# Performance work log

Measured on AMD Instinct MI355X. Metric: run time of the kernel, lower is better.

## Reference

```python
import jax, jax.numpy as jnp
import numpy as np

N = 100000   # nodes
E = 1600000  # edges (avg degree 16)
D = 128      # feature dim
L = 2        # nr_layers


def setup_inputs() -> dict:
    key = jax.random.key(0)
    k0, k1, k2, k3, k4 = jax.random.split(key, 5)
    x = jax.random.normal(k0, (N, D), dtype=jnp.float32)
    edge_index = jax.random.randint(k1, (2, E), 0, N, dtype=jnp.int32)
    edge_weight = jax.random.uniform(k2, (E,), dtype=jnp.float32)
    scale = 1.0 / np.sqrt(D)
    W_self = jax.random.normal(k3, (L, D, D), dtype=jnp.float32) * scale
    W_neigh = jax.random.normal(k4, (L, D, D), dtype=jnp.float32) * scale
    bias = jnp.zeros((L, D), dtype=jnp.float32)
    return {"x": x, "edge_index": edge_index, "edge_weight": edge_weight,
            "W_self": W_self, "W_neigh": W_neigh, "bias": bias}


def reference(x, edge_index, edge_weight, W_self, W_neigh, bias):
    src, dst = edge_index[0], edge_index[1]
    n = x.shape[0]
    # mean-aggregation denominator: number of incoming edges per node
    deg = jax.ops.segment_sum(jnp.ones_like(edge_weight), dst, num_segments=n)
    deg = jnp.maximum(deg, 1.0)[:, None]  # [N,1]
    nl = W_self.shape[0]
    for l in range(nl):
        msg = edge_weight[:, None] * x[src]                       # [E,D] gather
        agg = jax.ops.segment_sum(msg, dst, num_segments=n) / deg  # [N,D] scatter
        x = agg @ W_neigh[l] + x @ W_self[l] + bias[l]
        x = jax.nn.relu(x) if l < nl - 1 else jax.nn.sigmoid(x)
    return x
```

## Files before the change

### kernel.cpp

```cpp
#include <hip/hip_runtime.h>
#include <math.h>


#define D 128
#define BK_SHIFT 9
#define BK_NODES 512
#define CAP 10240
#define CH1 2048

typedef unsigned int uint;
typedef unsigned short ushort;
typedef __attribute__((ext_vector_type(2))) _Float16 h2;
typedef __attribute__((ext_vector_type(8))) _Float16 half8;
typedef __attribute__((ext_vector_type(4))) float f32x4;

__device__ __forceinline__ uint pkrtz(float lo, float hi) {
    auto v = __builtin_amdgcn_cvt_pkrtz(lo, hi);
    union { decltype(v) h; uint u; } c;
    c.h = v;
    return c.u;
}
__device__ __forceinline__ ushort f2h(float f) {
    return (ushort)(pkrtz(f, f) & 0xffffu);
}
__device__ __forceinline__ h2 u2h(uint u) {
    union { uint u; h2 h; } c;
    c.u = u;
    return c.h;
}
__device__ __forceinline__ uint h2u(h2 h) {
    union { h2 h; uint u; } c;
    c.h = h;
    return c.u;
}

__global__ __launch_bounds__(256) void k_prep(
    const float* __restrict__ x, uint* __restrict__ xh, int n8,
    const float* __restrict__ Wn, const float* __restrict__ Ws,
    ushort* __restrict__ wt, int wtotal,
    const int* __restrict__ src, const int* __restrict__ dst,
    const float* __restrict__ w, int E,
    int* __restrict__ bcur, int2* __restrict__ bedge,
    int nbSort, int nbConv)
{
    __shared__ int h[256];
    __shared__ int gbase[256];
    const int t = threadIdx.x;
    const int bid = blockIdx.x;

    if (bid >= nbSort) {
        int cb = bid - nbSort;
        if (cb < nbConv) {
            int i = cb * 256 + t;
            if (i >= n8) return;
            const float4* p = reinterpret_cast<const float4*>(x + (size_t)i * 8);
            float4 a = p[0], b = p[1];
            uint4 o;
            o.x = pkrtz(a.x, a.y);
            o.y = pkrtz(a.z, a.w);
            o.z = pkrtz(b.x, b.y);
            o.w = pkrtz(b.z, b.w);
            reinterpret_cast<uint4*>(xh)[i] = o;
        } else {
            int idx = (cb - nbConv) * 256 + t;
            if (idx >= wtotal) return;
            int l = idx >> 15;
            int j = (idx >> 8) & 127;
            int k = idx & 255;
            float v = (k < 128) ? Wn[(size_t)l * 16384 + (size_t)k * 128 + j]
                                : Ws[(size_t)l * 16384 + (size_t)(k - 128) * 128 + j];
            wt[idx] = f2h(v);
        }
        return;
    }

    h[t] = 0;
    __syncthreads();
    const int base0 = bid * CH1;
    uint pk[8]; float wr[8]; int br[8];
#pragma unroll
    for (int j = 0; j < 8; ++j) {
        int i = base0 + j * 256 + t;
        br[j] = -1;
        if (i < E) {
            int d = dst[i];
            int b = d >> BK_SHIFT;
            int r = atomicAdd(&h[b], 1);
            pk[j] = (uint)src[i] | ((uint)(d & (BK_NODES - 1)) << 17);
            wr[j] = w[i];
            br[j] = (b << 16) | r;
        }
    }
    __syncthreads();
    if (h[t] > 0) gbase[t] = atomicAdd(&bcur[t], h[t]);
    __syncthreads();
#pragma unroll
    for (int j = 0; j < 8; ++j) {
        if (br[j] >= 0) {
            int b = br[j] >> 16, r = br[j] & 0xffff;
            int slot = gbase[b] + r;
            if (slot < CAP)
                bedge[(size_t)b * CAP + slot] = make_int2((int)pk[j], __float_as_int(wr[j]));
        }
    }
}

__global__ __launch_bounds__(512) void k_sort2(
    const int2* __restrict__ bedge, const int* __restrict__ bcnt,
    int N, int2* __restrict__ rsdeg, int2* __restrict__ srcw)
{
    __shared__ int h[512];
    __shared__ int sa[512];
    __shared__ int sb[512];
    __shared__ int cur[512];
    const int t = threadIdx.x;
    const int b = blockIdx.x;
    const int gb = b * CAP;
    int cnt = bcnt[b];
    if (cnt > CAP) cnt = CAP;
    const int lo = b << BK_SHIFT;
    h[t] = 0;
    __syncthreads();
    for (int i = t; i < cnt; i += 512) {
        atomicAdd(&h[((uint)bedge[gb + i].x >> 17) & 511], 1);
    }
    __syncthreads();
    sa[t] = h[t];
    __syncthreads();
    int* sin = sa; int* sout = sb;
    for (int off = 1; off < 512; off <<= 1) {
        int v = sin[t];
        if (t >= off) v += sin[t - off];
        sout[t] = v;
        __syncthreads();
        int* tmp = sin; sin = sout; sout = tmp;
    }
    const int ex = sin[t] - h[t];
    cur[t] = ex;
    if (lo + t < N) rsdeg[lo + t] = make_int2(gb + ex, h[t]);
    __syncthreads();
    for (int i = t; i < cnt; i += 512) {
        int2 pe = bedge[gb + i];
        int n9 = ((uint)pe.x >> 17) & 511;
        int off = atomicAdd(&cur[n9], 1);
        float wv = __int_as_float(pe.y);
        srcw[gb + off] = make_int2((pe.x & 0x1FFFF) << 8, (int)pkrtz(wv, wv));
    }
}

__global__ __launch_bounds__(256, 8) void k_agg(
    const uint* __restrict__ xh,
    const int2* __restrict__ srcw,
    const int2* __restrict__ rsdeg,
    uint* __restrict__ agg, int N)
{
    const int tid = threadIdx.x;
    const int wv = tid >> 6;
    const int lane = tid & 63;
    const int node = blockIdx.x * 4 + wv;
    if (node >= N) return;
    const int q = lane >> 3;
    const int c8 = lane & 7;
    const int2 rd = rsdeg[node];
    const int st = rd.x;
    const int num = rd.y;
    const int en = st + num;

    h2 a2[8];
#pragma unroll
    for (int j = 0; j < 8; ++j) a2[j] = u2h(0u);

#pragma unroll 2
    for (int e = st + q; e < en; e += 8) {
        const int2 sw = srcw[e];
        const h2 w2 = u2h((uint)sw.y);
        const char* rowp = (const char*)xh + (uint)sw.x + (c8 << 5);
        const uint4 v0 = *reinterpret_cast<const uint4*>(rowp);
        const uint4 v1 = *reinterpret_cast<const uint4*>(rowp + 16);
        a2[0] = __builtin_elementwise_fma(w2, u2h(v0.x), a2[0]);
        a2[1] = __builtin_elementwise_fma(w2, u2h(v0.y), a2[1]);
        a2[2] = __builtin_elementwise_fma(w2, u2h(v0.z), a2[2]);
        a2[3] = __builtin_elementwise_fma(w2, u2h(v0.w), a2[3]);
        a2[4] = __builtin_elementwise_fma(w2, u2h(v1.x), a2[4]);
        a2[5] = __builtin_elementwise_fma(w2, u2h(v1.y), a2[5]);
        a2[6] = __builtin_elementwise_fma(w2, u2h(v1.z), a2[6]);
        a2[7] = __builtin_elementwise_fma(w2, u2h(v1.w), a2[7]);
    }

#pragma unroll
    for (int j = 0; j < 8; ++j) {
        a2[j] = a2[j] + u2h(__shfl_xor(h2u(a2[j]), 8));
        a2[j] = a2[j] + u2h(__shfl_xor(h2u(a2[j]), 16));
        a2[j] = a2[j] + u2h(__shfl_xor(h2u(a2[j]), 32));
    }

    if (q == 0) {
        const float invd = 1.0f / (float)(num > 1 ? num : 1);
        const h2 iv = u2h(pkrtz(invd, invd));
        uint4 o0, o1;
        o0.x = h2u(a2[0] * iv);
        o0.y = h2u(a2[1] * iv);
        o0.z = h2u(a2[2] * iv);
        o0.w = h2u(a2[3] * iv);
        o1.x = h2u(a2[4] * iv);
        o1.y = h2u(a2[5] * iv);
        o1.z = h2u(a2[6] * iv);
        o1.w = h2u(a2[7] * iv);
        uint* ar = agg + (size_t)node * 64 + c8 * 8;
        *reinterpret_cast<uint4*>(ar) = o0;
        *reinterpret_cast<uint4*>(ar + 4) = o1;
    }
}

template <int ACT, int OUTB>
__global__ __launch_bounds__(256) void k_gemm_mfma(
    const uint* __restrict__ aggh, const uint* __restrict__ xh,
    const uint* __restrict__ wt,
    const float* __restrict__ bias, void* __restrict__ xout, int N)
{
    const int tid = threadIdx.x;
    const int lane = tid & 63;
    const int wv = tid >> 6;
    const int wm = wv >> 1, wn = wv & 1;
    const int l16 = lane & 15;
    const int lq = lane >> 4;
    const int rowbase = blockIdx.x * 64 + wm * 32;
    const int colbase = wn * 64;

    half8 afrag[2][8];
#pragma unroll
    for (int mt = 0; mt < 2; ++mt) {
        int row = rowbase + mt * 16 + l16;
        if (row >= N) row = N - 1;
        const uint* arow = aggh + (size_t)row * 64;
        const uint* xrow = xh + (size_t)row * 64;
#pragma unroll
        for (int kk = 0; kk < 8; ++kk) {
            const uint* srcrow = (kk < 4) ? arow : xrow;
            uint4 u = *reinterpret_cast<const uint4*>(srcrow + (kk & 3) * 16 + lq * 4);
            afrag[mt][kk] = *reinterpret_cast<half8*>(&u);
        }
    }

#pragma unroll
    for (int nt = 0; nt < 4; ++nt) {
        const int col = colbase + nt * 16 + l16;
        const uint* wrow = wt + (size_t)col * 128;
        f32x4 acc0 = {0.f, 0.f, 0.f, 0.f};
        f32x4 acc1 = {0.f, 0.f, 0.f, 0.f};
#pragma unroll
        for (int kk = 0; kk < 8; ++kk) {
            uint4 u = *reinterpret_cast<const uint4*>(wrow + kk * 16 + lq * 4);
            half8 bfrag = *reinterpret_cast<half8*>(&u);
            acc0 = __builtin_amdgcn_mfma_f32_16x16x32_f16(afrag[0][kk], bfrag, acc0, 0, 0, 0);
            acc1 = __builtin_amdgcn_mfma_f32_16x16x32_f16(afrag[1][kk], bfrag, acc1, 0, 0, 0);
        }
        const float bv = bias[col];
#pragma unroll
        for (int mt = 0; mt < 2; ++mt) {
            const f32x4 acc = mt ? acc1 : acc0;
#pragma unroll
            for (int r = 0; r < 4; ++r) {
                int row = rowbase + mt * 16 + lq * 4 + r;
                if (row < N) {
                    float v = acc[r] + bv;
                    if (ACT == 0) v = fmaxf(v, 0.f);
                    else          v = 1.f / (1.f + __expf(-v));
                    if (OUTB) ((ushort*)xout)[(size_t)row * D + col] = f2h(v);
                    else      ((float*)xout)[(size_t)row * D + col] = v;
                }
            }
        }
    }
}

extern "C" void kernel_launch(void* const* d_in, const int* in_sizes, int n_in,
                              void* d_out, int out_size, void* d_ws, size_t ws_size,
                              hipStream_t stream) {
    const float* x      = (const float*)d_in[0];
    const int*   ei     = (const int*)d_in[1];
    const float* ew     = (const float*)d_in[2];
    const float* W_self = (const float*)d_in[3];
    const float* W_neigh= (const float*)d_in[4];
    const float* bias   = (const float*)d_in[5];
    float* out = (float*)d_out;

    const int N = in_sizes[0] / D;
    const int E = in_sizes[2];
    const int L = in_sizes[5] / D;
    const int B = (N + BK_NODES - 1) >> BK_SHIFT;

    const int* src = ei;
    const int* dst = ei + E;

    char* p = (char*)d_ws;
    auto carve = [&](size_t bytes) -> void* {
        void* r = (void*)p;
        p += (bytes + 255) & ~(size_t)255;
        return r;
    };
    int*   bcur   = (int*)carve(256 * 4);
    int2*  bedge  = (int2*)carve((size_t)B * CAP * 8);
    int2*  srcw   = (int2*)carve((size_t)B * CAP * 8);
    int2*  rsdeg  = (int2*)carve((size_t)N * 8);
    uint*  xh     = (uint*)carve((size_t)N * (D / 2) * 4);
    uint*  aggh   = (uint*)carve((size_t)N * (D / 2) * 4);
    uint*  hb     = (uint*)carve((size_t)N * (D / 2) * 4);
    uint*  wtbl   = (uint*)carve((size_t)L * 128 * 128 * 4);

    (void)hipMemsetAsync(bcur, 0, 256 * 4, stream);
    const int n8 = N * D / 8;
    const int wtotal = L * 32768;
    const int nbSort = (E + CH1 - 1) / CH1;
    const int nbConv = (n8 + 255) / 256;
    const int nbW = (wtotal + 255) / 256;
    k_prep<<<nbSort + nbConv + nbW, 256, 0, stream>>>(
        x, xh, n8, W_neigh, W_self, (ushort*)wtbl, wtotal,
        src, dst, ew, E, bcur, bedge, nbSort, nbConv);
    k_sort2<<<B, 512, 0, stream>>>(bedge, bcur, N, rsdeg, srcw);

    const int nblk_agg  = (N + 3) / 4;
    const int nblk_gemm = (N + 63) / 64;
    const uint* cur = xh;
    for (int l = 0; l < L; ++l) {
        const uint* wtl = wtbl + (size_t)l * 128 * 128;
        const float* bl = bias + (size_t)l * D;

        k_agg<<<nblk_agg, 256, 0, stream>>>(cur, srcw, rsdeg, aggh, N);
        if (l < L - 1) {
            k_gemm_mfma<0, 1><<<nblk_gemm, 256, 0, stream>>>(aggh, cur, wtl, bl, hb, N);
            cur = hb;
        } else {
            k_gemm_mfma<1, 0><<<nblk_gemm, 256, 0, stream>>>(aggh, cur, wtl, bl, out, N);
        }
    }
}
```

Before: 259.8 us.

## Split features into column-group planes and pack edge src/weight into one word

Stores node features and aggregates as 8 column-group planes of 16 halves each (N x 32 bytes per plane). The aggregation grid is split by column group, so each block gathers only a 3.2 MB plane, which can stay cache-resident while neighbors are fetched. Edge records are packed into 32 bits (17-bit source index plus 15-bit fp16 weight, sign dropped), halving the edge-list traffic, and the edge and degree loads now use nontemporal hints. In exchange, each gathered row segment is only 4 bytes per lane, the edge list is re-read once per column group (8 times per layer), and the GEMM reads and writes strided planar tiles.

```diff
diff --git a/kernel.cpp b/kernel.cpp
--- a/kernel.cpp
+++ b/kernel.cpp
@@ -35,7 +35,7 @@
 }
 
 __global__ __launch_bounds__(256) void k_prep(
-    const float* __restrict__ x, uint* __restrict__ xh, int n8,
+    const float* __restrict__ x, uint* __restrict__ xcs, int n8, int N,
     const float* __restrict__ Wn, const float* __restrict__ Ws,
     ushort* __restrict__ wt, int wtotal,
     const int* __restrict__ src, const int* __restrict__ dst,
@@ -60,7 +60,11 @@
             o.y = pkrtz(a.z, a.w);
             o.z = pkrtz(b.x, b.y);
             o.w = pkrtz(b.z, b.w);
-            reinterpret_cast<uint4*>(xh)[i] = o;
+            int row = i >> 4;
+            int pos8 = i & 15;
+            int cg = pos8 >> 1;
+            uint* dstp = xcs + ((size_t)cg * N + row) * 8 + (pos8 & 1) * 4;
+            *reinterpret_cast<uint4*>(dstp) = o;
         } else {
             int idx = (cb - nbConv) * 256 + t;
             if (idx >= wtotal) return;
@@ -107,7 +111,7 @@
 
 __global__ __launch_bounds__(512) void k_sort2(
     const int2* __restrict__ bedge, const int* __restrict__ bcnt,
-    int N, int2* __restrict__ rsdeg, int2* __restrict__ srcw)
+    int N, int2* __restrict__ rsdeg, uint* __restrict__ srcw)
 {
     __shared__ int h[512];
     __shared__ int sa[512];
@@ -144,77 +148,65 @@
         int n9 = ((uint)pe.x >> 17) & 511;
         int off = atomicAdd(&cur[n9], 1);
         float wv = __int_as_float(pe.y);
-        srcw[gb + off] = make_int2((pe.x & 0x1FFFF) << 8, (int)pkrtz(wv, wv));
+        uint wb = pkrtz(wv, wv) & 0x7FFFu;
+        srcw[gb + off] = ((uint)pe.x & 0x1FFFFu) | (wb << 17);
     }
 }
 
 __global__ __launch_bounds__(256, 8) void k_agg(
-    const uint* __restrict__ xh,
-    const int2* __restrict__ srcw,
+    const uint* __restrict__ xcs,
+    const uint* __restrict__ srcw,
     const int2* __restrict__ rsdeg,
-    uint* __restrict__ agg, int N)
+    uint* __restrict__ acs, int N)
 {
+    const int bid = blockIdx.x;
+    const int cg = bid & 7;
+    const int ng = bid >> 3;
     const int tid = threadIdx.x;
     const int wv = tid >> 6;
     const int lane = tid & 63;
-    const int node = blockIdx.x * 4 + wv;
-    if (node >= N) return;
     const int q = lane >> 3;
-    const int c8 = lane & 7;
-    const int2 rd = rsdeg[node];
-    const int st = rd.x;
-    const int num = rd.y;
-    const int en = st + num;
-
-    h2 a2[8];
-#pragma unroll
-    for (int j = 0; j < 8; ++j) a2[j] = u2h(0u);
-
+    const int c = lane & 7;
+    const char* xbase = (const char*)(xcs + (size_t)cg * N * 8) + (c << 2);
+    uint* obase = acs + (size_t)cg * N * 8;
+
+#pragma unroll
+    for (int i = 0; i < 4; ++i) {
+        const int node = ng * 16 + wv * 4 + i;
+        if (node >= N) break;
+        const long rdl = __builtin_nontemporal_load(
+            reinterpret_cast<const long*>(rsdeg + node));
+        const int st = (int)(rdl & 0xffffffffL);
+        const int num = (int)(rdl >> 32);
+        const int en = st + num;
+
+        h2 acc = u2h(0u);
 #pragma unroll 2
-    for (int e = st + q; e < en; e += 8) {
-        const int2 sw = srcw[e];
-        const h2 w2 = u2h((uint)sw.y);
-        const char* rowp = (const char*)xh + (uint)sw.x + (c8 << 5);
-        const uint4 v0 = *reinterpret_cast<const uint4*>(rowp);
-        const uint4 v1 = *reinterpret_cast<const uint4*>(rowp + 16);
-        a2[0] = __builtin_elementwise_fma(w2, u2h(v0.x), a2[0]);
-        a2[1] = __builtin_elementwise_fma(w2, u2h(v0.y), a2[1]);
-        a2[2] = __builtin_elementwise_fma(w2, u2h(v0.z), a2[2]);
-        a2[3] = __builtin_elementwise_fma(w2, u2h(v0.w), a2[3]);
-        a2[4] = __builtin_elementwise_fma(w2, u2h(v1.x), a2[4]);
-        a2[5] = __builtin_elementwise_fma(w2, u2h(v1.y), a2[5]);
-        a2[6] = __builtin_elementwise_fma(w2, u2h(v1.z), a2[6]);
-        a2[7] = __builtin_elementwise_fma(w2, u2h(v1.w), a2[7]);
-    }
-
-#pragma unroll
-    for (int j = 0; j < 8; ++j) {
-        a2[j] = a2[j] + u2h(__shfl_xor(h2u(a2[j]), 8));
-        a2[j] = a2[j] + u2h(__shfl_xor(h2u(a2[j]), 16));
-        a2[j] = a2[j] + u2h(__shfl_xor(h2u(a2[j]), 32));
-    }
-
-    if (q == 0) {
-        const float invd = 1.0f / (float)(num > 1 ? num : 1);
-        const h2 iv = u2h(pkrtz(invd, invd));
-        uint4 o0, o1;
-        o0.x = h2u(a2[0] * iv);
-        o0.y = h2u(a2[1] * iv);
-        o0.z = h2u(a2[2] * iv);
-        o0.w = h2u(a2[3] * iv);
-        o1.x = h2u(a2[4] * iv);
-        o1.y = h2u(a2[5] * iv);
-        o1.z = h2u(a2[6] * iv);
-        o1.w = h2u(a2[7] * iv);
-        uint* ar = agg + (size_t)node * 64 + c8 * 8;
-        *reinterpret_cast<uint4*>(ar) = o0;
-        *reinterpret_cast<uint4*>(ar + 4) = o1;
+        for (int e = st + q; e < en; e += 8) {
+            const uint v = __builtin_nontemporal_load(srcw + e);
+            const uint wu = v >> 17;
+            const h2 w2 = u2h(wu | (wu << 16));
+            const uint xv = *reinterpret_cast<const uint*>(
+                xbase + ((v & 0x1FFFFu) << 5));
+            acc = __builtin_elementwise_fma(w2, u2h(xv), acc);
+        }
+
+        acc = acc + u2h(__shfl_xor(h2u(acc), 8));
+        acc = acc + u2h(__shfl_xor(h2u(acc), 16));
+        acc = acc + u2h(__shfl_xor(h2u(acc), 32));
+
+        if (q == 0) {
+            const float invd = 1.0f / (float)(num > 1 ? num : 1);
+            const h2 iv = u2h(pkrtz(invd, invd));
+            __builtin_nontemporal_store(h2u(acc * iv),
+                                        obase + (size_t)node * 8 + c);
+        }
     }
 }
 
 template <int ACT, int OUTB>
 __global__ __launch_bounds__(256) void k_gemm_mfma(
-    const uint* __restrict__ aggh, const uint* __restrict__ xh,
+    const uint* __restrict__ acs, const uint* __restrict__ xcs,
     const uint* __restrict__ wt,
     const float* __restrict__ bias, void* __restrict__ xout, int N)
 {
@@ -232,12 +224,12 @@
     for (int mt = 0; mt < 2; ++mt) {
         int row = rowbase + mt * 16 + l16;
         if (row >= N) row = N - 1;
-        const uint* arow = aggh + (size_t)row * 64;
-        const uint* xrow = xh + (size_t)row * 64;
 #pragma unroll
         for (int kk = 0; kk < 8; ++kk) {
-            const uint* srcrow = (kk < 4) ? arow : xrow;
-            uint4 u = *reinterpret_cast<const uint4*>(srcrow + (kk & 3) * 16 + lq * 4);
+            const uint* srcb = (kk < 4) ? acs : xcs;
+            const int cgk = (kk & 3) * 2 + (lq >> 1);
+            uint4 u = *reinterpret_cast<const uint4*>(
+                srcb + ((size_t)cgk * N + row) * 8 + (lq & 1) * 4);
             afrag[mt][kk] = *reinterpret_cast<half8*>(&u);
         }
     }
@@ -256,6 +248,8 @@
             acc1 = __builtin_amdgcn_mfma_f32_16x16x32_f16(afrag[1][kk], bfrag, acc1, 0, 0, 0);
         }
         const float bv = bias[col];
+        const int cgo = col >> 4;
+        const int wo = col & 15;
 #pragma unroll
         for (int mt = 0; mt < 2; ++mt) {
             const f32x4 acc = mt ? acc1 : acc0;
@@ -266,7 +260,7 @@
                     float v = acc[r] + bv;
                     if (ACT == 0) v = fmaxf(v, 0.f);
                     else          v = 1.f / (1.f + __expf(-v));
-                    if (OUTB) ((ushort*)xout)[(size_t)row * D + col] = f2h(v);
+                    if (OUTB) ((ushort*)xout)[((size_t)cgo * N + row) * 16 + wo] = f2h(v);
                     else      ((float*)xout)[(size_t)row * D + col] = v;
                 }
             }
@@ -301,11 +295,11 @@
     };
     int*   bcur   = (int*)carve(256 * 4);
     int2*  bedge  = (int2*)carve((size_t)B * CAP * 8);
-    int2*  srcw   = (int2*)carve((size_t)B * CAP * 8);
+    uint*  srcw   = (uint*)carve((size_t)B * CAP * 4);
     int2*  rsdeg  = (int2*)carve((size_t)N * 8);
-    uint*  xh     = (uint*)carve((size_t)N * (D / 2) * 4);
-    uint*  aggh   = (uint*)carve((size_t)N * (D / 2) * 4);
-    uint*  hb     = (uint*)carve((size_t)N * (D / 2) * 4);
+    uint*  xcs    = (uint*)carve((size_t)N * 64 * 4);
+    uint*  acs    = (uint*)carve((size_t)N * 64 * 4);
+    uint*  hcs    = (uint*)carve((size_t)N * 64 * 4);
     uint*  wtbl   = (uint*)carve((size_t)L * 128 * 128 * 4);
 
     (void)hipMemsetAsync(bcur, 0, 256 * 4, stream);
@@ -315,23 +309,23 @@
     const int nbConv = (n8 + 255) / 256;
     const int nbW = (wtotal + 255) / 256;
     k_prep<<<nbSort + nbConv + nbW, 256, 0, stream>>>(
-        x, xh, n8, W_neigh, W_self, (ushort*)wtbl, wtotal,
+        x, xcs, n8, N, W_neigh, W_self, (ushort*)wtbl, wtotal,
         src, dst, ew, E, bcur, bedge, nbSort, nbConv);
     k_sort2<<<B, 512, 0, stream>>>(bedge, bcur, N, rsdeg, srcw);
 
-    const int nblk_agg  = (N + 3) / 4;
+    const int nblk_agg  = ((N + 15) / 16) * 8;
     const int nblk_gemm = (N + 63) / 64;
-    const uint* cur = xh;
+    const uint* cur = xcs;
     for (int l = 0; l < L; ++l) {
         const uint* wtl = wtbl + (size_t)l * 128 * 128;
         const float* bl = bias + (size_t)l * D;
 
-        k_agg<<<nblk_agg, 256, 0, stream>>>(cur, srcw, rsdeg, aggh, N);
+        k_agg<<<nblk_agg, 256, 0, stream>>>(cur, srcw, rsdeg, acs, N);
         if (l < L - 1) {
-            k_gemm_mfma<0, 1><<<nblk_gemm, 256, 0, stream>>>(aggh, cur, wtl, bl, hb, N);
-            cur = hb;
+            k_gemm_mfma<0, 1><<<nblk_gemm, 256, 0, stream>>>(acs, cur, wtl, bl, hcs, N);
+            cur = hcs;
         } else {
-            k_gemm_mfma<1, 0><<<nblk_gemm, 256, 0, stream>>>(aggh, cur, wtl, bl, out, N);
-        }
-    }
-}
+            k_gemm_mfma<1, 0><<<nblk_gemm, 256, 0, stream>>>(acs, cur, wtl, bl, out, N);
+        }
+    }
+}
```

After: 615.5 us. 2.37x slower.
